# Kernel tuning notes

Measured on AMD Instinct MI355X. Metric: run time of the kernel, lower is better.

Reference implementation:

```python
import jax, jax.numpy as jnp
import numpy as np

B, C, C2, E = 4, 1024, 1024, 1024
D = 1024          # context_size (d_q = d_kv)
NH = 16           # module's n_heads arg -> actual head_dim after the quirky view
G = D // NH       # effective number of head groups = 64


def setup_inputs() -> dict:
    key = jax.random.key(0)
    ks = jax.random.split(key, 6)
    s = 0.02
    return {
        "x1": jax.random.normal(ks[0], (B, C, E), dtype=jnp.float32),
        "x2": jax.random.normal(ks[1], (B, C2, E), dtype=jnp.float32),
        "W_q": jax.random.normal(ks[2], (E, D), dtype=jnp.float32) * s,
        "W_k": jax.random.normal(ks[3], (E, D), dtype=jnp.float32) * s,
        "W_v": jax.random.normal(ks[4], (E, D), dtype=jnp.float32) * s,
        "W_o": jax.random.normal(ks[5], (D, D), dtype=jnp.float32) * s,
    }


def _split_heads(t):
    # (B, S, D) -> view (B, S, G, NH) -> transpose(1,2) -> (B, G, S, NH)
    b, s, _ = t.shape
    return jnp.transpose(t.reshape(b, s, G, NH), (0, 2, 1, 3))


def reference(x1, x2, W_q, W_k, W_v, W_o):
    Q = _split_heads(x1 @ W_q)   # (B, G, C, NH)
    K = _split_heads(x2 @ W_k)   # (B, G, C2, NH)
    V = _split_heads(x2 @ W_v)   # (B, G, C2, NH)
    scale = 1.0 / jnp.sqrt(jnp.asarray(NH, dtype=Q.dtype))
    scores = jnp.einsum("bgqh,bgkh->bgqk", Q, K) * scale  # (B, G, C, C2)
    w = jax.nn.softmax(scores, axis=-1)
    out = jnp.einsum("bgqk,bgkh->bgqh", w, V)             # (B, G, C, NH)
    out = jnp.transpose(out, (0, 2, 1, 3)).reshape(B, C, D)
    return out @ W_o  # dropout p=0 -> identity
```

## Files before the change

kernel.cpp:

```cpp
#include <hip/hip_runtime.h>


typedef _Float16 f16x8 __attribute__((ext_vector_type(8)));
typedef _Float16 f16x4 __attribute__((ext_vector_type(4)));
typedef _Float16 f16x2 __attribute__((ext_vector_type(2)));
typedef float    f32x4 __attribute__((ext_vector_type(4)));
typedef float    f32x16 __attribute__((ext_vector_type(16)));

#define GLOAD_LDS16(gp, lp)                                              \
    __builtin_amdgcn_global_load_lds(                                    \
        (const __attribute__((address_space(1))) void*)(gp),             \
        (__attribute__((address_space(3))) void*)(lp), 16, 0, 0)

static __device__ __forceinline__ f16x8 pack8f(const float* p) {
    f16x2 a = __builtin_bit_cast(f16x2, __builtin_amdgcn_cvt_pkrtz(p[0], p[1]));
    f16x2 b = __builtin_bit_cast(f16x2, __builtin_amdgcn_cvt_pkrtz(p[2], p[3]));
    f16x2 c = __builtin_bit_cast(f16x2, __builtin_amdgcn_cvt_pkrtz(p[4], p[5]));
    f16x2 d = __builtin_bit_cast(f16x2, __builtin_amdgcn_cvt_pkrtz(p[6], p[7]));
    f16x8 r;
    r[0] = a[0]; r[1] = a[1]; r[2] = b[0]; r[3] = b[1];
    r[4] = c[0]; r[5] = c[1]; r[6] = d[0]; r[7] = d[1];
    return r;
}

__global__ __launch_bounds__(256) void prep_kernel(
        const float* __restrict__ x1, const float* __restrict__ x2,
        const float* __restrict__ W0, const float* __restrict__ W1,
        const float* __restrict__ W2, const float* __restrict__ W3,
        _Float16* __restrict__ y1, _Float16* __restrict__ y2,
        _Float16* __restrict__ T0, _Float16* __restrict__ T1,
        _Float16* __restrict__ T2, _Float16* __restrict__ T3) {
    int bx = blockIdx.x, tid = threadIdx.x;
    if (bx < 8192) {
        int i = bx * 256 + tid;
        const float* x = (i < 1048576) ? x1 : x2;
        _Float16* y = (i < 1048576) ? y1 : y2;
        int j = i & 1048575;
        float4 v = ((const float4*)x)[j];
        f16x4 h = { (_Float16)v.x, (_Float16)v.y, (_Float16)v.z, (_Float16)v.w };
        ((f16x4*)y)[j] = h;
    } else {
        int z = (bx - 8192) >> 10;
        const float* W = (z == 0) ? W0 : (z == 1) ? W1 : (z == 2) ? W2 : W3;
        _Float16* WT = (z == 0) ? T0 : (z == 1) ? T1 : (z == 2) ? T2 : T3;
        int t = (bx - 8192) & 1023;
        int c0 = (t & 31) * 32, r0 = (t >> 5) * 32;
        __shared__ float tile[32][33];
        int tx = tid & 31, ty = tid >> 5;
#pragma unroll
        for (int i = 0; i < 32; i += 8)
            tile[ty + i][tx] = W[(r0 + ty + i) * 1024 + (c0 + tx)];
        __syncthreads();
#pragma unroll
        for (int i = 0; i < 32; i += 8)
            WT[(c0 + ty + i) * 1024 + (r0 + tx)] = (_Float16)tile[tx][ty + i];
    }
}

template <bool OUTF32>
static __device__ __forceinline__ void gemm_body(const _Float16* __restrict__ A,
                                                 const _Float16* __restrict__ BT,
                                                 void* __restrict__ Cout,
                                                 _Float16* As, _Float16* Bs) {
    const int tid = threadIdx.x, lane = tid & 63, wave = tid >> 6;
    const int wm = wave >> 1, wn = wave & 1;
    const int col = lane & 15, quad = lane >> 4;
    const int m0 = blockIdx.y * 128, n0 = blockIdx.x * 128;

    f32x4 acc[4][4];
#pragma unroll
    for (int i = 0; i < 4; i++)
#pragma unroll
        for (int j = 0; j < 4; j++) acc[i][j] = (f32x4){0.f, 0.f, 0.f, 0.f};

    const int srow = wave * 8 + (lane >> 3);
    const int sch = (lane & 7) * 8;
    const _Float16* Ag = A + (size_t)(m0 + srow) * 1024 + sch;
    const _Float16* Bg = BT + (size_t)(n0 + srow) * 1024 + sch;
    _Float16* Asl = As + wave * 512;
    _Float16* Bsl = Bs + wave * 512;

    for (int kt = 0; kt < 16; kt++) {
        __syncthreads();
#pragma unroll
        for (int c = 0; c < 4; c++) {
            GLOAD_LDS16(Ag + (size_t)(c * 32) * 1024 + kt * 64, Asl + c * 2048);
            GLOAD_LDS16(Bg + (size_t)(c * 32) * 1024 + kt * 64, Bsl + c * 2048);
        }
        __syncthreads();
#pragma unroll
        for (int ki = 0; ki < 2; ki++) {
            f16x8 af[4], bf[4];
#pragma unroll
            for (int i = 0; i < 4; i++)
                af[i] = *(const f16x8*)(As + (wm * 64 + i * 16 + col) * 64 + ki * 32 + quad * 8);
#pragma unroll
            for (int j = 0; j < 4; j++)
                bf[j] = *(const f16x8*)(Bs + (wn * 64 + j * 16 + col) * 64 + ki * 32 + quad * 8);
#pragma unroll
            for (int i = 0; i < 4; i++)
#pragma unroll
                for (int j = 0; j < 4; j++)
                    acc[i][j] = __builtin_amdgcn_mfma_f32_16x16x32_f16(af[i], bf[j], acc[i][j], 0, 0, 0);
        }
    }

#pragma unroll
    for (int i = 0; i < 4; i++)
#pragma unroll
        for (int ii = 0; ii < 4; ii++) {
            int row = m0 + wm * 64 + i * 16 + quad * 4 + ii;
#pragma unroll
            for (int j = 0; j < 4; j++) {
                int cc = n0 + wn * 64 + j * 16 + col;
                if (OUTF32) ((float*)Cout)[(size_t)row * 1024 + cc] = acc[i][j][ii];
                else ((_Float16*)Cout)[(size_t)row * 1024 + cc] = (_Float16)acc[i][j][ii];
            }
        }
}

__global__ __launch_bounds__(256, 3) void gemm_qkv_kernel(
        const _Float16* __restrict__ x1h, const _Float16* __restrict__ x2h,
        const _Float16* __restrict__ WqT, const _Float16* __restrict__ WkT,
        const _Float16* __restrict__ WvT,
        _Float16* __restrict__ Qh, _Float16* __restrict__ Kh, _Float16* __restrict__ Vh) {
    __shared__ _Float16 As[128 * 64], Bs[128 * 64];
    int z = blockIdx.z;
    const _Float16* A = (z == 0) ? x1h : x2h;
    const _Float16* BT = (z == 0) ? WqT : (z == 1) ? WkT : WvT;
    _Float16* C = (z == 0) ? Qh : (z == 1) ? Kh : Vh;
    gemm_body<false>(A, BT, (void*)C, As, Bs);
}

__global__ __launch_bounds__(256, 3) void gemm_wo_kernel(const _Float16* __restrict__ Ah,
                                                         const _Float16* __restrict__ WoT,
                                                         float* __restrict__ out) {
    __shared__ _Float16 As[128 * 64], Bs[128 * 64];
    gemm_body<true>(Ah, WoT, (void*)out, As, Bs);
}

__global__ __launch_bounds__(512, 4) void attn_kernel(const _Float16* __restrict__ Qh,
                                                      const _Float16* __restrict__ Kh,
                                                      const _Float16* __restrict__ Vh,
                                                      _Float16* __restrict__ Ah) {
    int pair = blockIdx.y;
    int b = pair >> 6, g = pair & 63;
    __shared__ _Float16 KA[8192];
    __shared__ _Float16 VA[8192];
    __shared__ _Float16 ones[8];

    const _Float16* Kg = Kh + (size_t)(b * 1024) * 1024 + g * 16;
    const _Float16* Vg = Vh + (size_t)(b * 1024) * 1024 + g * 16;
    int tid = threadIdx.x;
    if (tid < 8) ones[tid] = (_Float16)1.f;

    int lane = tid & 63, wave = tid >> 6;
    int n = lane & 31, h5 = lane >> 5;
    int q0 = blockIdx.x * 512 + wave * 64;

    f16x8 qf[2];
#pragma unroll
    for (int qg = 0; qg < 2; qg++) {
        f16x8 t = *(const f16x8*)(Qh + (size_t)(b * 1024 + q0 + qg * 32 + n) * 1024 +
                                  g * 16 + h5 * 8);
#pragma unroll
        for (int j = 0; j < 8; j++) qf[qg][j] = (_Float16)((float)t[j] * 0.360673760f);
    }

    f32x16 acc[2];
#pragma unroll
    for (int qg = 0; qg < 2; qg++)
        acc[qg] = (f32x16){0.f, 0.f, 0.f, 0.f, 0.f, 0.f, 0.f, 0.f,
                           0.f, 0.f, 0.f, 0.f, 0.f, 0.f, 0.f, 0.f};
    const f32x16 zero16 = acc[0];
    const _Float16* vbase = (n < 16) ? (VA + (n + 16 * h5) * 8) : ones;
    const int vstep = (n < 16) ? 256 : 0;

    for (int c = 0; c < 2; c++) {
        if (c) __syncthreads();
#pragma unroll
        for (int it = 0; it < 2; it++) {
            int row = it * 256 + (tid >> 1);
            int part = tid & 1;
            int pm = (row & 19) | ((row & 4) << 1) | ((row & 8) >> 1);
            *(uint4*)(KA + (((row >> 5) * 64) + pm + 32 * part) * 8) =
                *(const uint4*)(Kg + (size_t)(c * 512 + row) * 1024 + part * 8);
        }
#pragma unroll
        for (int it = 0; it < 2; it++) {
            int row = it * 256 + (tid >> 1);
            int part = tid & 1;
            f16x8 v = *(const f16x8*)(Vg + (size_t)(c * 512 + row) * 1024 + part * 8);
            int base = (row >> 4) * 256 + ((row >> 3) & 1) * 128 + part * 64 + (row & 7);
#pragma unroll
            for (int j = 0; j < 8; j++) VA[base + j * 8] = v[j];
        }
        __syncthreads();

#pragma unroll 2
        for (int t = 0; t < 16; t++) {
            f16x8 ak = *(const f16x8*)(KA + (t * 64 + lane) * 8);
            f16x8 av0 = *(const f16x8*)(vbase + (2 * t) * vstep);
            f16x8 av1 = *(const f16x8*)(vbase + (2 * t + 1) * vstep);
#pragma unroll
            for (int qg = 0; qg < 2; qg++) {
                f32x16 s = __builtin_amdgcn_mfma_f32_32x32x16_f16(ak, qf[qg], zero16, 0, 0, 0);
                float p[16];
#pragma unroll
                for (int i = 0; i < 16; i++) p[i] = __builtin_amdgcn_exp2f(s[i]);
                f16x8 pb0 = pack8f(p);
                f16x8 pb1 = pack8f(p + 8);
                acc[qg] = __builtin_amdgcn_mfma_f32_32x32x16_f16(av0, pb0, acc[qg], 0, 0, 0);
                acc[qg] = __builtin_amdgcn_mfma_f32_32x32x16_f16(av1, pb1, acc[qg], 0, 0, 0);
            }
        }
    }

#pragma unroll
    for (int qg = 0; qg < 2; qg++) {
        float rl = 1.0f / acc[qg][8];
        f16x4 o0, o1;
#pragma unroll
        for (int i = 0; i < 4; i++) o0[i] = (_Float16)(acc[qg][i] * rl);
#pragma unroll
        for (int i = 0; i < 4; i++) o1[i] = (_Float16)(acc[qg][4 + i] * rl);
        _Float16* ob = Ah + (size_t)(b * 1024 + q0 + qg * 32 + n) * 1024 + g * 16 + h5 * 4;
        *(f16x4*)(ob) = o0;
        *(f16x4*)(ob + 8) = o1;
    }
}

extern "C" void kernel_launch(void* const* d_in, const int* in_sizes, int n_in,
                              void* d_out, int out_size, void* d_ws, size_t ws_size,
                              hipStream_t stream) {
    const float* x1 = (const float*)d_in[0];
    const float* x2 = (const float*)d_in[1];
    const float* Wq = (const float*)d_in[2];
    const float* Wk = (const float*)d_in[3];
    const float* Wv = (const float*)d_in[4];
    const float* Wo = (const float*)d_in[5];

    char* ws = (char*)d_ws;
    const size_t MB = 1u << 20;
    if (ws_size < 56 * MB) return;

    _Float16* x1h = (_Float16*)(ws + 0 * MB);
    _Float16* x2h = (_Float16*)(ws + 8 * MB);
    _Float16* WqT = (_Float16*)(ws + 16 * MB);
    _Float16* WkT = (_Float16*)(ws + 18 * MB);
    _Float16* WvT = (_Float16*)(ws + 20 * MB);
    _Float16* WoT = (_Float16*)(ws + 22 * MB);
    _Float16* Qh  = (_Float16*)(ws + 24 * MB);
    _Float16* Kh  = (_Float16*)(ws + 32 * MB);
    _Float16* Vh  = (_Float16*)(ws + 40 * MB);
    _Float16* Ah  = (_Float16*)(ws + 48 * MB);

    prep_kernel<<<12288, 256, 0, stream>>>(x1, x2, Wq, Wk, Wv, Wo,
                                           x1h, x2h, WqT, WkT, WvT, WoT);

    gemm_qkv_kernel<<<dim3(8, 32, 3), 256, 0, stream>>>(x1h, x2h, WqT, WkT, WvT, Qh, Kh, Vh);

    attn_kernel<<<dim3(2, 256), 512, 0, stream>>>(Qh, Kh, Vh, Ah);

    gemm_wo_kernel<<<dim3(8, 32), 256, 0, stream>>>(Ah, WoT, (float*)d_out);
}
```

Baseline: 198.0 us.

## Fuse K/V projection GEMM tiles, shrink Wo tile and attention blocks

The QKV GEMM now uses a 1D grid in which the K and V projections share one concatenated transposed weight (WkT and WvT laid out contiguously), so x2 row tiles are grouped across both outputs. The Wo GEMM drops to 64-row tiles to launch 512 blocks and raise occupancy. The attention kernel now runs 256-thread blocks over 256 queries each with a higher occupancy bound. The aim is better L2 reuse and wave fill across the 256 CUs. The trade-off is that K/V tiles are reloaded more often, and the code depends on WkT and WvT being adjacent in the workspace.

```diff
diff --git a/kernel.cpp b/kernel.cpp
--- a/kernel.cpp
+++ b/kernel.cpp
@@ -57,48 +57,49 @@
     }
 }
 
-template <bool OUTF32>
-static __device__ __forceinline__ void gemm_body(const _Float16* __restrict__ A,
-                                                 const _Float16* __restrict__ BT,
-                                                 void* __restrict__ Cout,
+template <int MT, bool OUTF32>
+static __device__ __forceinline__ void gemm_body(const _Float16* __restrict__ Atile,
+                                                 const _Float16* __restrict__ BTtile,
+                                                 void* __restrict__ Ctile,
                                                  _Float16* As, _Float16* Bs) {
+    constexpr int AF = MT / 32;
     const int tid = threadIdx.x, lane = tid & 63, wave = tid >> 6;
     const int wm = wave >> 1, wn = wave & 1;
     const int col = lane & 15, quad = lane >> 4;
-    const int m0 = blockIdx.y * 128, n0 = blockIdx.x * 128;
-
-    f32x4 acc[4][4];
-#pragma unroll
-    for (int i = 0; i < 4; i++)
+
+    f32x4 acc[AF][4];
+#pragma unroll
+    for (int i = 0; i < AF; i++)
 #pragma unroll
         for (int j = 0; j < 4; j++) acc[i][j] = (f32x4){0.f, 0.f, 0.f, 0.f};
 
     const int srow = wave * 8 + (lane >> 3);
     const int sch = (lane & 7) * 8;
-    const _Float16* Ag = A + (size_t)(m0 + srow) * 1024 + sch;
-    const _Float16* Bg = BT + (size_t)(n0 + srow) * 1024 + sch;
+    const _Float16* Ag = Atile + (size_t)srow * 1024 + sch;
+    const _Float16* Bg = BTtile + (size_t)srow * 1024 + sch;
     _Float16* Asl = As + wave * 512;
     _Float16* Bsl = Bs + wave * 512;
 
     for (int kt = 0; kt < 16; kt++) {
         __syncthreads();
 #pragma unroll
-        for (int c = 0; c < 4; c++) {
+        for (int c = 0; c < AF; c++)
             GLOAD_LDS16(Ag + (size_t)(c * 32) * 1024 + kt * 64, Asl + c * 2048);
+#pragma unroll
+        for (int c = 0; c < 4; c++)
             GLOAD_LDS16(Bg + (size_t)(c * 32) * 1024 + kt * 64, Bsl + c * 2048);
-        }
         __syncthreads();
 #pragma unroll
         for (int ki = 0; ki < 2; ki++) {
-            f16x8 af[4], bf[4];
-#pragma unroll
-            for (int i = 0; i < 4; i++)
-                af[i] = *(const f16x8*)(As + (wm * 64 + i * 16 + col) * 64 + ki * 32 + quad * 8);
+            f16x8 af[AF], bf[4];
+#pragma unroll
+            for (int i = 0; i < AF; i++)
+                af[i] = *(const f16x8*)(As + (wm * (MT / 2) + i * 16 + col) * 64 + ki * 32 + quad * 8);
 #pragma unroll
             for (int j = 0; j < 4; j++)
                 bf[j] = *(const f16x8*)(Bs + (wn * 64 + j * 16 + col) * 64 + ki * 32 + quad * 8);
 #pragma unroll
-            for (int i = 0; i < 4; i++)
+            for (int i = 0; i < AF; i++)
 #pragma unroll
                 for (int j = 0; j < 4; j++)
                     acc[i][j] = __builtin_amdgcn_mfma_f32_16x16x32_f16(af[i], bf[j], acc[i][j], 0, 0, 0);
@@ -106,40 +107,53 @@
     }
 
 #pragma unroll
-    for (int i = 0; i < 4; i++)
+    for (int i = 0; i < AF; i++)
 #pragma unroll
         for (int ii = 0; ii < 4; ii++) {
-            int row = m0 + wm * 64 + i * 16 + quad * 4 + ii;
+            int row = wm * (MT / 2) + i * 16 + quad * 4 + ii;
 #pragma unroll
             for (int j = 0; j < 4; j++) {
-                int cc = n0 + wn * 64 + j * 16 + col;
-                if (OUTF32) ((float*)Cout)[(size_t)row * 1024 + cc] = acc[i][j][ii];
-                else ((_Float16*)Cout)[(size_t)row * 1024 + cc] = (_Float16)acc[i][j][ii];
+                int cc = wn * 64 + j * 16 + col;
+                if (OUTF32) ((float*)Ctile)[(size_t)row * 1024 + cc] = acc[i][j][ii];
+                else ((_Float16*)Ctile)[(size_t)row * 1024 + cc] = (_Float16)acc[i][j][ii];
             }
         }
 }
 
 __global__ __launch_bounds__(256, 3) void gemm_qkv_kernel(
         const _Float16* __restrict__ x1h, const _Float16* __restrict__ x2h,
-        const _Float16* __restrict__ WqT, const _Float16* __restrict__ WkT,
-        const _Float16* __restrict__ WvT,
+        const _Float16* __restrict__ WqT, const _Float16* __restrict__ WkvT,
         _Float16* __restrict__ Qh, _Float16* __restrict__ Kh, _Float16* __restrict__ Vh) {
     __shared__ _Float16 As[128 * 64], Bs[128 * 64];
-    int z = blockIdx.z;
-    const _Float16* A = (z == 0) ? x1h : x2h;
-    const _Float16* BT = (z == 0) ? WqT : (z == 1) ? WkT : WvT;
-    _Float16* C = (z == 0) ? Qh : (z == 1) ? Kh : Vh;
-    gemm_body<false>(A, BT, (void*)C, As, Bs);
-}
-
-__global__ __launch_bounds__(256, 3) void gemm_wo_kernel(const _Float16* __restrict__ Ah,
+    int gx = blockIdx.x;
+    const _Float16 *A, *BT;
+    _Float16* C;
+    int m0, n0;
+    if (gx < 256) {
+        m0 = (gx >> 3) * 128; n0 = (gx & 7) * 128;
+        A = x1h; BT = WqT + (size_t)n0 * 1024; C = Qh + n0;
+    } else {
+        int idx = gx - 256;
+        m0 = (idx >> 4) * 128;
+        int nb = idx & 15;
+        n0 = nb * 128;
+        A = x2h; BT = WkvT + (size_t)n0 * 1024;
+        C = (nb < 8) ? (Kh + n0) : (Vh + (n0 - 1024));
+    }
+    gemm_body<128, false>(A + (size_t)m0 * 1024, BT, (void*)(C + (size_t)m0 * 1024), As, Bs);
+}
+
+__global__ __launch_bounds__(256, 4) void gemm_wo_kernel(const _Float16* __restrict__ Ah,
                                                          const _Float16* __restrict__ WoT,
                                                          float* __restrict__ out) {
-    __shared__ _Float16 As[128 * 64], Bs[128 * 64];
-    gemm_body<true>(Ah, WoT, (void*)out, As, Bs);
-}
-
-__global__ __launch_bounds__(512, 4) void attn_kernel(const _Float16* __restrict__ Qh,
+    __shared__ _Float16 As[64 * 64], Bs[128 * 64];
+    int gx = blockIdx.x;
+    int m0 = (gx >> 3) * 64, n0 = (gx & 7) * 128;
+    gemm_body<64, true>(Ah + (size_t)m0 * 1024, WoT + (size_t)n0 * 1024,
+                        (void*)(out + (size_t)m0 * 1024 + n0), As, Bs);
+}
+
+__global__ __launch_bounds__(256, 8) void attn_kernel(const _Float16* __restrict__ Qh,
                                                       const _Float16* __restrict__ Kh,
                                                       const _Float16* __restrict__ Vh,
                                                       _Float16* __restrict__ Ah) {
@@ -156,7 +170,7 @@
 
     int lane = tid & 63, wave = tid >> 6;
     int n = lane & 31, h5 = lane >> 5;
-    int q0 = blockIdx.x * 512 + wave * 64;
+    int q0 = blockIdx.x * 256 + wave * 64;
 
     f16x8 qf[2];
 #pragma unroll
@@ -179,16 +193,16 @@
     for (int c = 0; c < 2; c++) {
         if (c) __syncthreads();
 #pragma unroll
-        for (int it = 0; it < 2; it++) {
-            int row = it * 256 + (tid >> 1);
+        for (int it = 0; it < 4; it++) {
+            int row = it * 128 + (tid >> 1);
             int part = tid & 1;
             int pm = (row & 19) | ((row & 4) << 1) | ((row & 8) >> 1);
             *(uint4*)(KA + (((row >> 5) * 64) + pm + 32 * part) * 8) =
                 *(const uint4*)(Kg + (size_t)(c * 512 + row) * 1024 + part * 8);
         }
 #pragma unroll
-        for (int it = 0; it < 2; it++) {
-            int row = it * 256 + (tid >> 1);
+        for (int it = 0; it < 4; it++) {
+            int row = it * 128 + (tid >> 1);
             int part = tid & 1;
             f16x8 v = *(const f16x8*)(Vg + (size_t)(c * 512 + row) * 1024 + part * 8);
             int base = (row >> 4) * 256 + ((row >> 3) & 1) * 128 + part * 64 + (row & 7);
@@ -258,9 +272,9 @@
     prep_kernel<<<12288, 256, 0, stream>>>(x1, x2, Wq, Wk, Wv, Wo,
                                            x1h, x2h, WqT, WkT, WvT, WoT);
 
-    gemm_qkv_kernel<<<dim3(8, 32, 3), 256, 0, stream>>>(x1h, x2h, WqT, WkT, WvT, Qh, Kh, Vh);
-
-    attn_kernel<<<dim3(2, 256), 512, 0, stream>>>(Qh, Kh, Vh, Ah);
-
-    gemm_wo_kernel<<<dim3(8, 32), 256, 0, stream>>>(Ah, WoT, (float*)d_out);
-}
+    gemm_qkv_kernel<<<768, 256, 0, stream>>>(x1h, x2h, WqT, WkT, Qh, Kh, Vh);
+
+    attn_kernel<<<dim3(4, 256), 256, 0, stream>>>(Qh, Kh, Vh, Ah);
+
+    gemm_wo_kernel<<<512, 256, 0, stream>>>(Ah, WoT, (float*)d_out);
+}
```

New measurement: 197.4 us. About the same (-0.3%).
